# Performance work log

Measured on AMD Instinct MI355X. Metric: run time of the kernel, lower is better.

The kernel has to match this reference:

```python
import jax, jax.numpy as jnp
import numpy as np

D = 10000          # hypervector dimensionality (DIMENSIONS in source)
ALPHA = 0.85
MAX_ITER = 100
TOL = 1e-6


def _pagerank(edge_index, num_nodes):
    # sparse column-stochastic adjacency power iteration (faithful to source)
    row, col = edge_index[0], edge_index[1]
    ones = jnp.ones(edge_index.shape[1], dtype=jnp.float32)
    deg = jax.ops.segment_sum(ones, col, num_segments=num_nodes)  # bincount(columns)
    vals = ALPHA / deg[col]                                       # alpha / out-degree per edge
    p = jnp.float32(1.0 / num_nodes)

    def cond(state):
        v, err, i = state
        return jnp.logical_and(i < MAX_ITER, err >= num_nodes * TOL)

    def body(state):
        v, _, i = state
        mv = jax.ops.segment_sum(vals * v[col], row, num_segments=num_nodes)
        v_new = mv + p * (1.0 - ALPHA)
        return (v_new, jnp.abs(v_new - v).sum(), i + 1)

    v0 = jnp.full((num_nodes,), p, dtype=jnp.float32)
    v, _, _ = jax.lax.while_loop(cond, body, (v0, jnp.float32(jnp.inf), jnp.int32(0)))
    return v


def _undirected_unique(edge_index, num_nodes):
    # to_undirected: sort each edge's endpoints then unique columns.
    # jit-safe emulation: sort by scalar key, mask duplicate keys (weight 0).
    ei = jnp.sort(edge_index, axis=0)                 # [2, E], min/max per edge
    keys = ei[0] * num_nodes + ei[1]
    order = jnp.argsort(keys)
    ksort = keys[order]
    first = jnp.concatenate([jnp.ones((1,), bool), ksort[1:] != ksort[:-1]])
    mask = first.astype(jnp.float32)                  # 1.0 for unique edges, 0.0 for dups
    return ei[0][order], ei[1][order], mask


def setup_inputs() -> dict:
    key = jax.random.key(0)
    k1, k2, k3 = jax.random.split(key, 3)
    N, E, C = 2000, 8192, 10
    edge_index = jax.random.randint(k1, (2, E), 0, N, dtype=jnp.int64)
    # torchhd Random embedding: random bipolar {-1, +1} hypervectors
    node_ids_weight = jnp.where(jax.random.uniform(k2, (N, D)) < 0.5, -1.0, 1.0).astype(jnp.float32)
    # source inits classify weight to 0; use small random values so the output is non-degenerate
    classify_weight = jax.random.normal(k3, (C, D), dtype=jnp.float32) * 0.01
    return {"edge_index": edge_index, "node_ids_weight": node_ids_weight,
            "classify_weight": classify_weight, "num_nodes": N}


def reference(edge_index, node_ids_weight, classify_weight, num_nodes):
    pr = _pagerank(edge_index, num_nodes)
    pr_argsort = jnp.argsort(pr)
    # node_id_hvs[pr_argsort] = node_ids.weight[:num_nodes]
    node_id_hvs = jnp.zeros((num_nodes, D), dtype=node_ids_weight.dtype)
    node_id_hvs = node_id_hvs.at[pr_argsort].set(node_ids_weight[:num_nodes])
    row, col, mask = _undirected_unique(edge_index, num_nodes)
    # bind = elementwise multiply (MAP VSA); multiset = sum over (unique) edges
    enc = jnp.einsum('e,ed,ed->d', mask, node_id_hvs[row], node_id_hvs[col])
    return enc @ classify_weight.T   # Linear(D, num_classes, bias=False)
```

## Files before the change

kernel.cpp:

```cpp
#include <hip/hip_runtime.h>
#include <hip/hip_bf16.h>

#define NN 2000
#define NE 8192
#define DIM 10000
#define NCLS 10
#define HASH_SZ 32768
#define WORDS 313
#define ECH 8
#define RBLK 64
#define REGD 12
#define DUMMY 2047

#define WS_K       0
#define WS_ENC     64
#define WS_V       328576
#define WS_RANK    336576
#define WS_PAIRS   344576
#define WS_HASH    377344
#define WS_PACK    508416

#define ZERO_BYTES 40128
#define ZERO_VEC  (ZERO_BYTES / 16)
#define HASH_VEC  (HASH_SZ * 4 / 16)
#define INIT_TOT  (ZERO_VEC + HASH_VEC)
#define FUSE_ITEMS (INIT_TOT + NN * WORDS)
#define FUSE_BLK  ((FUSE_ITEMS + 1023) / 1024)

__device__ __forceinline__ float wave_sum_dpp(float x) {
#define DPPADD(ctrl, rm, bm)                                                     \
  {                                                                              \
    int y_ = __builtin_amdgcn_update_dpp(0, __float_as_int(x), ctrl, rm, bm, false); \
    x = __fadd_rn(x, __int_as_float(y_));                                        \
  }
  DPPADD(0x111, 0xF, 0xF);
  DPPADD(0x112, 0xF, 0xF);
  DPPADD(0x114, 0xF, 0xE);
  DPPADD(0x118, 0xF, 0xC);
  DPPADD(0x142, 0xA, 0xF);
  DPPADD(0x143, 0xC, 0xF);
#undef DPPADD
  return x;
}

__global__ __launch_bounds__(1024) void fused_pre_kernel(const int* __restrict__ eidx,
                                                         const float* __restrict__ W,
                                                         char* __restrict__ ws) {
  if (blockIdx.x != 0) {
    int t = (int)(blockIdx.x - 1) * 1024 + threadIdx.x;
    if (t < ZERO_VEC) {
      reinterpret_cast<uint4*>(ws)[t] = make_uint4(0u, 0u, 0u, 0u);
      return;
    }
    if (t < INIT_TOT) {
      reinterpret_cast<uint4*>(ws + WS_HASH)[t - ZERO_VEC] =
          make_uint4(0xFFFFFFFFu, 0xFFFFFFFFu, 0xFFFFFFFFu, 0xFFFFFFFFu);
      return;
    }
    int j = t - INIT_TOT;
    if (j >= NN * WORDS) return;
    unsigned int* packed = (unsigned int*)(ws + WS_PACK);
    int w = j / NN;
    int node = j - w * NN;
    int d0 = w * 32;
    const float* p = W + (size_t)node * DIM + d0;
    unsigned int m = 0;
    if (d0 + 32 <= DIM) {
#pragma unroll
      for (int q = 0; q < 8; ++q) {
        float4 v4 = *reinterpret_cast<const float4*>(p + q * 4);
        m |= (__float_as_uint(v4.x) >> 31) << (q * 4);
        m |= (__float_as_uint(v4.y) >> 31) << (q * 4 + 1);
        m |= (__float_as_uint(v4.z) >> 31) << (q * 4 + 2);
        m |= (__float_as_uint(v4.w) >> 31) << (q * 4 + 3);
      }
    } else {
      for (int q = 0; q < DIM - d0; ++q) m |= (__float_as_uint(p[q]) >> 31) << q;
    }
    packed[(size_t)w * NN + node] = m;
    return;
  }

  __shared__ unsigned short s_ccol[NE];
  __shared__ unsigned short s_ced[NE];
  __shared__ int s_base[NN + 1];
  __shared__ int s_aux[2048];
  __shared__ int s_w[2048];
  __shared__ float s_wv[2][2048];
  __shared__ float s_red[2][16];
  float* s_val = (float*)s_aux;

  int tid = threadIdx.x;
  int wid = tid >> 6, lane = tid & 63;

  for (int i = tid; i < 2048; i += 1024) { s_w[i] = 0; s_aux[i] = 0; }
  for (int i = NN + tid; i < 2048; i += 1024) { s_wv[0][i] = 0.f; s_wv[1][i] = 0.f; }
  __syncthreads();

  int er[8], ec[8];
#pragma unroll
  for (int k = 0; k < 8; ++k) {
    int e = tid + k * 1024;
    er[k] = eidx[e];
    ec[k] = eidx[NE + e];
    atomicAdd(&s_w[er[k]], 1);
    atomicAdd(&s_aux[ec[k]], 1);
  }
  __syncthreads();

  {
    int n0 = tid, n1 = tid + 1024;
    for (int st = 1; st < 2048; st <<= 1) {
      int v0 = (n0 >= st) ? s_w[n0 - st] : 0;
      int v1 = (n1 >= st) ? s_w[n1 - st] : 0;
      __syncthreads();
      s_w[n0] += v0;
      s_w[n1] += v1;
      __syncthreads();
    }
    if (tid == 0) s_base[0] = 0;
    for (int n = tid; n < NN; n += 1024) s_base[n + 1] = s_w[n];
  }
  __syncthreads();
  for (int i = tid; i < 2048; i += 1024) s_w[i] = 0;
  __syncthreads();

#pragma unroll
  for (int k = 0; k < 8; ++k) {
    int e = tid + k * 1024;
    int r = er[k];
    int slot = s_base[r] + atomicAdd(&s_w[r], 1);
    s_ccol[slot] = (unsigned short)ec[k];
    s_ced[slot] = (unsigned short)e;
  }
  __syncthreads();

  const float p = 0.0005f;
  const float addv = 0.0005f * 0.15f;
  for (int n = tid; n < NN; n += 1024) {
    int s0 = s_base[n], s1 = s_base[n + 1];
    for (int a = s0 + 1; a < s1; ++a) {
      unsigned short ke = s_ced[a], kc = s_ccol[a];
      int b = a - 1;
      while (b >= s0 && s_ced[b] > ke) {
        s_ced[b + 1] = s_ced[b];
        s_ccol[b + 1] = s_ccol[b];
        --b;
      }
      s_ced[b + 1] = ke;
      s_ccol[b + 1] = kc;
    }
    float vv = 0.85f / (float)s_aux[n];
    s_val[n] = vv;
    s_wv[0][n] = __fmul_rn(vv, p);
  }
  __syncthreads();

  int b0s = s_base[tid], b0e = s_base[tid + 1];
  int b1s = 0, b1e = 0;
  bool has1 = (tid + 1024 < NN);
  if (has1) { b1s = s_base[tid + 1024]; b1e = s_base[tid + 1025]; }
  float val0 = s_val[tid];
  float val1 = has1 ? s_val[tid + 1024] : 0.f;
  int c0r[REGD], c1r[REGD];
#pragma unroll
  for (int k = 0; k < REGD; ++k) {
    int i0 = b0s + k;
    c0r[k] = (i0 < b0e) ? (int)s_ccol[min(i0, NE - 1)] : DUMMY;
    int i1 = b1s + k;
    c1r[k] = (has1 && i1 < b1e) ? (int)s_ccol[min(i1, NE - 1)] : DUMMY;
  }
  float vc0 = p, vc1 = p;

  float err = __builtin_inff();
  int it = 0;
  int pb = 0;
  while (it < 100 && err >= 0.002f) {
    const float* wv = s_wv[pb];
    float ep = 0.f;
    float sum = 0.f;
#pragma unroll
    for (int k = 0; k < REGD; ++k) sum = __fadd_rn(sum, wv[c0r[k]]);
    for (int k = b0s + REGD; k < b0e; ++k) sum = __fadd_rn(sum, wv[s_ccol[k]]);
    float vn0 = __fadd_rn(sum, addv);
    ep += fabsf(__fsub_rn(vn0, vc0));
    float vn1 = vc1;
    if (has1) {
      sum = 0.f;
#pragma unroll
      for (int k = 0; k < REGD; ++k) sum = __fadd_rn(sum, wv[c1r[k]]);
      for (int k = b1s + REGD; k < b1e; ++k) sum = __fadd_rn(sum, wv[s_ccol[k]]);
      vn1 = __fadd_rn(sum, addv);
      ep += fabsf(__fsub_rn(vn1, vc1));
    }
    float* wvn = s_wv[pb ^ 1];
    wvn[tid] = __fmul_rn(val0, vn0);
    if (has1) wvn[tid + 1024] = __fmul_rn(val1, vn1);
    vc0 = vn0; vc1 = vn1;
    float wsum = wave_sum_dpp(ep);
    if (lane == 63) s_red[pb][wid] = wsum;
    __syncthreads();
    float t = 0.f;
#pragma unroll
    for (int w2 = 0; w2 < 16; ++w2) t += s_red[pb][w2];
    err = t;
    pb ^= 1;
    ++it;
  }
  float* vout = (float*)(ws + WS_V);
  vout[tid] = vc0;
  if (has1) vout[tid + 1024] = vc1;
}

__global__ __launch_bounds__(256) void rank_dedup_kernel(const int* __restrict__ eidx,
                                                         char* __restrict__ ws) {
  int tid = threadIdx.x;
  if (blockIdx.x < 32) {
    const float* v = (const float*)(ws + WS_V);
    int* rnk = (int*)(ws + WS_RANK);
    __shared__ float s_v[NN];
    __shared__ int s_part[4][RBLK];
    for (int j = tid; j < NN; j += 256) s_v[j] = v[j];
    __syncthreads();
    int li = tid & (RBLK - 1);
    int seg = tid >> 6;
    int i = blockIdx.x * RBLK + li;
    float vi = (i < NN) ? s_v[i] : 0.f;
    const int jper = NN / 4;
    int j0 = seg * jper, j1 = j0 + jper;
    int r = 0;
    for (int j = j0; j < j1; ++j) {
      float vj = s_v[j];
      r += ((vj < vi) || (vj == vi && j < i)) ? 1 : 0;
    }
    s_part[seg][li] = r;
    __syncthreads();
    if (tid < RBLK) {
      int i2 = blockIdx.x * RBLK + tid;
      if (i2 < NN)
        rnk[i2] = s_part[0][tid] + s_part[1][tid] + s_part[2][tid] + s_part[3][tid];
    }
  } else {
    int* hash = (int*)(ws + WS_HASH);
    unsigned int* pairs = (unsigned int*)(ws + WS_PAIRS);
    int* Kp = (int*)(ws + WS_K);
    int e = (int)(blockIdx.x - 32) * 256 + tid;
    int r = eidx[e], c = eidx[NE + e];
    int a = min(r, c), b = max(r, c);
    int key = a * NN + b;
    unsigned int h = ((unsigned int)key * 2654435761u) >> 17;
    for (;;) {
      h &= (HASH_SZ - 1);
      int old = atomicCAS(&hash[h], -1, key);
      if (old == -1) {
        int idx = atomicAdd(Kp, 1);
        pairs[idx] = ((unsigned int)a << 16) | (unsigned int)b;
        return;
      }
      if (old == key) return;
      ++h;
    }
  }
}

__global__ __launch_bounds__(256) void encpop_kernel(char* __restrict__ ws) {
  const unsigned int* packed = (const unsigned int*)(ws + WS_PACK);
  const unsigned int* pairs = (const unsigned int*)(ws + WS_PAIRS);
  const int* Kp = (const int*)(ws + WS_K);
  const int* rnk_g = (const int*)(ws + WS_RANK);
  int* enc_int = (int*)(ws + WS_ENC);
  __shared__ unsigned short s_rnk[NN];
  __shared__ unsigned int s_col[NN];
  __shared__ int s_part[4][32];
  int w = blockIdx.x;
  int tid = threadIdx.x;
  int wid = tid >> 6, lane = tid & 63;
  for (int i = tid; i < NN; i += 256) s_rnk[i] = (unsigned short)rnk_g[i];
  __syncthreads();
  for (int i = tid; i < NN; i += 256)
    s_col[i] = packed[(size_t)w * NN + s_rnk[i]];
  __syncthreads();
  int K = *Kp;
  const int per = NE / ECH;
  int e0 = blockIdx.y * per;
  int cnt[32];
#pragma unroll
  for (int b = 0; b < 32; ++b) cnt[b] = 0;
  for (int e = e0 + tid; e < e0 + per; e += 256) {
    unsigned int x = 0;
    if (e < K) {
      unsigned int pk = pairs[e];
      x = s_col[pk >> 16] ^ s_col[pk & 0xffffu];
    }
#pragma unroll
    for (int b = 0; b < 32; ++b)
      cnt[b] += (int)__popcll(__ballot(x & (1u << b)));
  }
  if (lane == 0) {
#pragma unroll
    for (int b = 0; b < 32; ++b) s_part[wid][b] = cnt[b];
  }
  __syncthreads();
  if (tid < 32) {
    int tot = s_part[0][tid] + s_part[1][tid] + s_part[2][tid] + s_part[3][tid];
    if (tot) atomicAdd(&enc_int[w * 32 + tid], tot);
  }
}

__global__ __launch_bounds__(256) void out_kernel(const float* __restrict__ Wc,
                                                  char* __restrict__ ws,
                                                  float* __restrict__ out) {
  const int* enc_int = (const int*)(ws + WS_ENC);
  int K = *(const int*)(ws + WS_K);
  __shared__ float red[4];
  int c = blockIdx.x;
  float s = 0.f;
  for (int d = threadIdx.x; d < DIM; d += 256)
    s += (float)(K - 2 * enc_int[d]) * Wc[c * DIM + d];
  for (int o = 32; o > 0; o >>= 1) s += __shfl_down(s, o, 64);
  if ((threadIdx.x & 63) == 0) red[threadIdx.x >> 6] = s;
  __syncthreads();
  if (threadIdx.x == 0) out[c] = red[0] + red[1] + red[2] + red[3];
}

extern "C" void kernel_launch(void* const* d_in, const int* in_sizes, int n_in,
                              void* d_out, int out_size, void* d_ws, size_t ws_size,
                              hipStream_t stream) {
  const int* eidx = (const int*)d_in[0];
  const float* Wn = (const float*)d_in[1];
  const float* Wc = (const float*)d_in[2];
  float* out = (float*)d_out;
  char* ws = (char*)d_ws;

  fused_pre_kernel<<<FUSE_BLK + 1, 1024, 0, stream>>>(eidx, Wn, ws);
  rank_dedup_kernel<<<64, 256, 0, stream>>>(eidx, ws);
  encpop_kernel<<<dim3(WORDS, ECH), 256, 0, stream>>>(ws);
  out_kernel<<<NCLS, 256, 0, stream>>>(Wc, ws, out);
}
```

Baseline: 87.07 us.

## Sort PageRank nodes by in-degree so waves skip unused gather slots

Builds a counting-sort permutation of nodes by in-edge count using wave ballots and shared-memory prefix sums, then assigns nodes to threads in that order. Each wave computes its maximum register-resident degree and exits the unrolled gather loop early. This cuts wasted shared-memory loads of the dummy slot for low-degree nodes in every power iteration. The cost is extra setup work and barriers, plus scattered writes into the shared vector.

```diff
diff --git a/kernel.cpp b/kernel.cpp
--- a/kernel.cpp
+++ b/kernel.cpp
@@ -88,6 +88,7 @@
   __shared__ int s_w[2048];
   __shared__ float s_wv[2][2048];
   __shared__ float s_red[2][16];
+  __shared__ int s_colsum[32], s_off2[32];
   float* s_val = (float*)s_aux;
 
   int tid = threadIdx.x;
@@ -156,20 +157,78 @@
   }
   __syncthreads();
 
-  int b0s = s_base[tid], b0e = s_base[tid + 1];
+  unsigned short* s_perm = s_ced;
+  {
+    int nA = tid, nB = tid + 1024;
+    int dA = s_base[nA + 1] - s_base[nA];
+    int kA = min(dA, 31);
+    int kB = 63;
+    if (nB < NN) kB = min(s_base[nB + 1] - s_base[nB], 31);
+    int g0 = tid >> 6, g1 = 16 + (tid >> 6);
+    unsigned long long lt = (1ull << lane) - 1ull;
+    int rA = 0, rB = 0;
+#pragma unroll
+    for (int d = 0; d < 32; ++d) {
+      unsigned long long mA = __ballot(kA == d);
+      if (kA == d) rA = (int)__popcll(mA & lt);
+      if (lane == d) s_w[g0 * 32 + d] = (int)__popcll(mA);
+      unsigned long long mB = __ballot(kB == d);
+      if (kB == d) rB = (int)__popcll(mB & lt);
+      if (lane == d) s_w[g1 * 32 + d] = (int)__popcll(mB);
+    }
+    __syncthreads();
+    if (tid < 32) {
+      int cs = 0;
+      for (int g = 0; g < 32; ++g) cs += s_w[g * 32 + tid];
+      s_colsum[tid] = cs;
+    }
+    __syncthreads();
+    if (tid < 32) {
+      int off = 0;
+      for (int d = tid + 1; d < 32; ++d) off += s_colsum[d];
+      s_off2[tid] = off;
+    }
+    {
+      int g = tid >> 5, d = tid & 31;
+      int go = 0;
+      for (int gp = 0; gp < g; ++gp) go += s_w[gp * 32 + d];
+      __syncthreads();
+      s_w[1024 + tid] = go;
+    }
+    __syncthreads();
+    int posA = s_off2[kA] + s_w[1024 + g0 * 32 + kA] + rA;
+    s_perm[posA] = (unsigned short)nA;
+    if (nB < NN) {
+      int posB = s_off2[kB] + s_w[1024 + g1 * 32 + kB] + rB;
+      s_perm[posB] = (unsigned short)nB;
+    }
+  }
+  __syncthreads();
+
+  int p0 = s_perm[tid];
+  bool has1 = (tid + 1024 < NN);
+  int p1 = has1 ? (int)s_perm[tid + 1024] : 0;
+  int b0s = s_base[p0], b0e = s_base[p0 + 1];
   int b1s = 0, b1e = 0;
-  bool has1 = (tid + 1024 < NN);
-  if (has1) { b1s = s_base[tid + 1024]; b1e = s_base[tid + 1025]; }
-  float val0 = s_val[tid];
-  float val1 = has1 ? s_val[tid + 1024] : 0.f;
+  if (has1) { b1s = s_base[p1]; b1e = s_base[p1 + 1]; }
+  int deg0 = b0e - b0s, deg1 = b1e - b1s;
+  float val0 = s_val[p0];
+  float val1 = has1 ? s_val[p1] : 0.f;
   int c0r[REGD], c1r[REGD];
 #pragma unroll
   for (int k = 0; k < REGD; ++k) {
-    int i0 = b0s + k;
-    c0r[k] = (i0 < b0e) ? (int)s_ccol[min(i0, NE - 1)] : DUMMY;
-    int i1 = b1s + k;
-    c1r[k] = (has1 && i1 < b1e) ? (int)s_ccol[min(i1, NE - 1)] : DUMMY;
-  }
+    c0r[k] = (k < deg0) ? (int)s_ccol[b0s + k] : DUMMY;
+    c1r[k] = (has1 && k < deg1) ? (int)s_ccol[b1s + k] : DUMMY;
+  }
+  int wd0 = min(deg0, REGD);
+  int wd1 = has1 ? min(deg1, REGD) : 0;
+#pragma unroll
+  for (int o = 32; o > 0; o >>= 1) {
+    wd0 = max(wd0, __shfl_xor(wd0, o, 64));
+    wd1 = max(wd1, __shfl_xor(wd1, o, 64));
+  }
+  int wmax0 = __builtin_amdgcn_readfirstlane(wd0);
+  int wmax1 = __builtin_amdgcn_readfirstlane(wd1);
   float vc0 = p, vc1 = p;
 
   float err = __builtin_inff();
@@ -180,7 +239,10 @@
     float ep = 0.f;
     float sum = 0.f;
 #pragma unroll
-    for (int k = 0; k < REGD; ++k) sum = __fadd_rn(sum, wv[c0r[k]]);
+    for (int k = 0; k < REGD; ++k) {
+      if (k >= wmax0) break;
+      sum = __fadd_rn(sum, wv[c0r[k]]);
+    }
     for (int k = b0s + REGD; k < b0e; ++k) sum = __fadd_rn(sum, wv[s_ccol[k]]);
     float vn0 = __fadd_rn(sum, addv);
     ep += fabsf(__fsub_rn(vn0, vc0));
@@ -188,14 +250,17 @@
     if (has1) {
       sum = 0.f;
 #pragma unroll
-      for (int k = 0; k < REGD; ++k) sum = __fadd_rn(sum, wv[c1r[k]]);
+      for (int k = 0; k < REGD; ++k) {
+        if (k >= wmax1) break;
+        sum = __fadd_rn(sum, wv[c1r[k]]);
+      }
       for (int k = b1s + REGD; k < b1e; ++k) sum = __fadd_rn(sum, wv[s_ccol[k]]);
       vn1 = __fadd_rn(sum, addv);
       ep += fabsf(__fsub_rn(vn1, vc1));
     }
     float* wvn = s_wv[pb ^ 1];
-    wvn[tid] = __fmul_rn(val0, vn0);
-    if (has1) wvn[tid + 1024] = __fmul_rn(val1, vn1);
+    wvn[p0] = __fmul_rn(val0, vn0);
+    if (has1) wvn[p1] = __fmul_rn(val1, vn1);
     vc0 = vn0; vc1 = vn1;
     float wsum = wave_sum_dpp(ep);
     if (lane == 63) s_red[pb][wid] = wsum;
@@ -208,8 +273,8 @@
     ++it;
   }
   float* vout = (float*)(ws + WS_V);
-  vout[tid] = vc0;
-  if (has1) vout[tid + 1024] = vc1;
+  vout[p0] = vc0;
+  if (has1) vout[p1] = vc1;
 }
 
 __global__ __launch_bounds__(256) void rank_dedup_kernel(const int* __restrict__ eidx,
```

Measured after the change: 87.60 us. No clear change (+0.6%).
